# Kernel tuning notes

Measured on AMD Instinct MI355X. Metric: run time of the kernel, lower is better.

The kernel has to match this reference:

```python
import jax, jax.numpy as jnp
import numpy as np

DIM_IN = 512
DIM_OUT = 64


def setup_inputs() -> dict:
    key = jax.random.key(0)
    kx, kq, kk, kv = jax.random.split(key, 4)
    x = jax.random.normal(kx, (4, 4096, DIM_IN), dtype=jnp.float32)
    s = 1.0 / np.sqrt(DIM_IN)
    # torch nn.Linear stores weight as [out, in]; keep same convention
    Wq = jax.random.uniform(kq, (DIM_OUT, DIM_IN), jnp.float32, -s, s)
    Wk = jax.random.uniform(kk, (DIM_OUT, DIM_IN), jnp.float32, -s, s)
    Wv = jax.random.uniform(kv, (DIM_OUT, DIM_IN), jnp.float32, -s, s)
    return {"x": x, "Wq": Wq, "Wk": Wk, "Wv": Wv}


def reference(x, Wq, Wk, Wv):
    # q/k/v projections: [B,S,Din] @ [Din,Dout] -> [B,S,Dout]
    q = jnp.einsum("bsd,od->bso", x, Wq)
    k = jnp.einsum("bsd,od->bso", x, Wk)
    v = jnp.einsum("bsd,od->bso", x, Wv)
    scale = 1.0 / jnp.sqrt(jnp.asarray(q.shape[-1], q.dtype))
    scores = jnp.einsum("bqo,bko->bqk", q, k) * scale  # [B,S,S]
    weights = jax.nn.softmax(scores, axis=-1)
    out = jnp.einsum("bqk,bko->bqo", weights, v)  # [B,S,Dout]
    return out
```

## Files before the change

kernel.cpp:

```cpp
#include <hip/hip_runtime.h>
#include <hip/hip_bf16.h>

#define SEQ 4096
#define MTOT 16384

typedef float f32x4  __attribute__((ext_vector_type(4)));
typedef float f32x16 __attribute__((ext_vector_type(16)));
typedef _Float16 f16;
typedef _Float16 f16x4 __attribute__((ext_vector_type(4)));
typedef _Float16 f16x8 __attribute__((ext_vector_type(8)));
typedef unsigned int   u32;
typedef unsigned int   u32x2 __attribute__((ext_vector_type(2)));
typedef unsigned short u16;

static constexpr size_t QL_B   = 0;
static constexpr size_t KL_B   = 2u << 20;
static constexpr size_t VL_B   = 4u << 20;
static constexpr size_t WL_B   = 6u << 20;
static constexpr size_t PART_B = 8u << 20;
static constexpr size_t ML_B   = 42u << 20;

__device__ __forceinline__ u16 h16(float v) { return __builtin_bit_cast(u16, (f16)v); }
__device__ __forceinline__ u32 pkrtz(float a, float b) {
  return __builtin_bit_cast(u32, __builtin_amdgcn_cvt_pkrtz(a, b));
}
__device__ __forceinline__ void gl16(const u16* g, u16* l) {
  __builtin_amdgcn_global_load_lds((const __attribute__((address_space(1))) void*)g,
                                   (__attribute__((address_space(3))) void*)l, 16, 0, 0);
}

__global__ __launch_bounds__(256) void wconv_kernel(const float* __restrict__ Wq,
                                                    const float* __restrict__ Wk,
                                                    const float* __restrict__ Wv,
                                                    u16* __restrict__ wlin) {
  const float QSC = 0.18033688011112042f;
  int e = blockIdx.x * 256 + threadIdx.x;
  int flat = e * 4;
  int colg = flat >> 9;
  int k0   = flat & 511;
  int mat  = colg >> 6;
  const float* W = (mat == 0) ? Wq : (mat == 1 ? Wk : Wv);
  f32x4 v = *(const f32x4*)(W + (size_t)(colg & 63) * 512 + k0);
  if (mat == 0) v *= QSC;
  int s = colg >> 4, r16 = colg & 15;
  int step = k0 >> 5, g = (k0 & 31) >> 3, jb = k0 & 7;
  __attribute__((aligned(8))) u16 b[4];
#pragma unroll
  for (int j = 0; j < 4; ++j) b[j] = h16(v[j]);
  *(uint2*)(wlin + ((size_t)(s * 16 + step) * 64 + g * 16 + r16) * 8 + jb) = *(uint2*)b;
}

__global__ __launch_bounds__(256, 4) void proj_kernel(const float* __restrict__ x,
                                                      const u16* __restrict__ wlin,
                                                      u16* __restrict__ ws) {
  __shared__ __attribute__((aligned(16))) u16 xl[8192];
  float* scr = (float*)xl;

  const int tid  = threadIdx.x;
  const int blk  = blockIdx.x;
  const int lane = tid & 63;
  const int ng   = tid >> 6;
  const int r16  = lane & 15;
  const int g    = lane >> 4;
  const int m0   = blk * 16;

#pragma unroll
  for (int i = 0; i < 8; ++i) {
    int f = tid * 4 + i * 1024;
    int row = f >> 9, k0 = f & 511;
    f32x4 v = *(const f32x4*)(x + (size_t)m0 * 512 + f);
    __attribute__((aligned(8))) u16 b[4];
#pragma unroll
    for (int j = 0; j < 4; ++j) b[j] = h16(v[j]);
    int ln = ((k0 & 31) >> 3) * 16 + row;
    *(uint2*)(xl + ((size_t)(k0 >> 5) * 64 + ln) * 8 + (k0 & 7)) = *(uint2*)b;
  }
  __syncthreads();

  f32x4 acc[3];
#pragma unroll
  for (int s = 0; s < 3; ++s) acc[s] = (f32x4){0.f, 0.f, 0.f, 0.f};

#pragma unroll 2
  for (int step = 0; step < 16; ++step) {
    f16x8 a = *(const f16x8*)(xl + ((size_t)step * 64 + lane) * 8);
#pragma unroll
    for (int s = 0; s < 3; ++s) {
      int sg = ng * 3 + s;
      f16x8 b = *(const f16x8*)(wlin + ((size_t)(sg * 16 + step) * 64 + lane) * 8);
      acc[s] = __builtin_amdgcn_mfma_f32_16x16x32_f16(a, b, acc[s], 0, 0, 0);
    }
  }
  __syncthreads();

#pragma unroll
  for (int s = 0; s < 3; ++s)
#pragma unroll
    for (int rr = 0; rr < 4; ++rr)
      scr[(g * 4 + rr) * 193 + ng * 48 + s * 16 + r16] = acc[s][rr];
  __syncthreads();

  u16* Ql = ws + (QL_B >> 1);
  u16* Kl = ws + (KL_B >> 1);
  u16* Vl = ws + (VL_B >> 1);
  const int batch = m0 >> 12;
  const int tile  = (m0 >> 5) & 127;
  const int half  = (m0 >> 4) & 1;

  {
    int t2 = tid & 127;
    int r  = t2 & 15, hh = (t2 >> 4) & 1, ch = t2 >> 5;
    int l31 = half * 16 + r;
    __attribute__((aligned(16))) u16 b[8];
    if (tid < 128) {
#pragma unroll
      for (int j = 0; j < 8; ++j) b[j] = h16(scr[r * 193 + 64 + ch * 16 + hh * 8 + j]);
      *(uint4*)(Kl + ((size_t)((batch * 128 + tile) * 4 + ch) * 64 + hh * 32 + l31) * 8) =
          *(uint4*)b;
    } else {
#pragma unroll
      for (int j = 0; j < 8; ++j) b[j] = h16(scr[r * 193 + ch * 16 + hh * 8 + j]);
      int qhalf = (m0 >> 5);
      *(uint4*)(Ql + ((size_t)(qhalf * 4 + ch) * 64 + hh * 32 + l31) * 8) = *(uint4*)b;
    }
  }
  {
    int z = tid & 1, l31 = (tid >> 1) & 31, hh = (tid >> 6) & 1, db = tid >> 7;
    int d = db * 32 + l31;
    __attribute__((aligned(8))) u16 b[4];
#pragma unroll
    for (int j = 0; j < 4; ++j) b[j] = h16(scr[(8 * z + 4 * hh + j) * 193 + 128 + d]);
    *(uint2*)(Vl + ((size_t)(((batch * 128 + tile) * 2 + db) * 2 + half) * 64 + hh * 32 + l31) *
                       8 + z * 4) = *(uint2*)b;
  }
}

__global__ __launch_bounds__(512, 4) void attn_kernel(u16* __restrict__ ws) {
  __shared__ __attribute__((aligned(16))) u16 kvb[2][8192];

  const int tid  = threadIdx.x;
  const int w    = tid >> 6;
  const int lane = tid & 63;
  const int l31  = lane & 31;
  const int h    = lane >> 5;
  const int bx   = blockIdx.x;
  const int qb   = bx >> 3;
  const int sp   = bx & 7;
  const int bb   = qb >> 4;
  const int q0   = qb * 256 + w * 32;

  const u16* Ql = ws + (QL_B >> 1);
  const u16* Kl = ws + (KL_B >> 1);
  const u16* Vl = ws + (VL_B >> 1);

  const int qhalf = qb * 8 + w;
  f16x8 qf[4];
#pragma unroll
  for (int ch = 0; ch < 4; ++ch)
    qf[ch] = *(const f16x8*)(Ql + ((size_t)(qhalf * 4 + ch) * 64 + lane) * 8);

  f32x16 oacc[2];
#pragma unroll
  for (int db = 0; db < 2; ++db)
#pragma unroll
    for (int r = 0; r < 16; ++r) oacc[db][r] = 0.f;
  float mrun = -INFINITY, lrun = 0.f;
  const float RTHR = 11.0f;

  const int kt0 = bb * 128 + sp * 16;

  auto stage = [&](int b, int p) {
#pragma unroll
    for (int cc = 0; cc < 2; ++cc) {
      const int c = w * 2 + cc;
      const u16* src;
      if (c < 8) {
        src = Kl + (size_t)(kt0 + p * 2 + (c >> 2)) * 2048 + (c & 3) * 512 + lane * 8;
      } else {
        const int c2 = c - 8;
        src = Vl + (size_t)(kt0 + p * 2 + (c2 >> 2)) * 2048 + (c2 & 3) * 512 + lane * 8;
      }
      gl16(src, &kvb[b][c * 512]);
    }
  };

  stage(0, 0);
  __syncthreads();

#pragma unroll 1
  for (int p = 0; p < 8; ++p) {
    const int cur = p & 1;
    if (p < 7) stage(cur ^ 1, p + 1);

#pragma unroll
    for (int s = 0; s < 2; ++s) {
      f16x8 ka[4], vp[2][2];
#pragma unroll
      for (int ch = 0; ch < 4; ++ch)
        ka[ch] = *(const f16x8*)&kvb[cur][((s << 2) + ch) * 512 + lane * 8];
#pragma unroll
      for (int db = 0; db < 2; ++db)
#pragma unroll
        for (int pp = 0; pp < 2; ++pp)
          vp[db][pp] = *(const f16x8*)&kvb[cur][(8 + (s << 2) + db * 2 + pp) * 512 + lane * 8];

      f32x16 sac;
#pragma unroll
      for (int r = 0; r < 16; ++r) sac[r] = 0.f;
#pragma unroll
      for (int ch = 0; ch < 4; ++ch)
        sac = __builtin_amdgcn_mfma_f32_32x32x16_f16(ka[ch], qf[ch], sac, 0, 0, 0);

      float mt = sac[0];
#pragma unroll
      for (int r = 1; r < 16; ++r) mt = fmaxf(mt, sac[r]);
      if (__any(mt > mrun + RTHR)) {
        float mtw  = fmaxf(mt, __shfl_xor(mt, 32));
        float nm   = fmaxf(mrun, mtw);
        float corr = exp2f(mrun - nm);
        lrun *= corr;
        mrun = nm;
#pragma unroll
        for (int db = 0; db < 2; ++db)
#pragma unroll
          for (int r = 0; r < 16; ++r) oacc[db][r] *= corr;
      }
#pragma unroll
      for (int r = 0; r < 16; ++r) {
        float pv = exp2f(sac[r] - mrun);
        sac[r] = pv;
        lrun += pv;
      }

      f16x4 pb[4];
#pragma unroll
      for (int c = 0; c < 4; ++c) {
        u32x2 pk;
        pk[0] = pkrtz(sac[4 * c + 0], sac[4 * c + 1]);
        pk[1] = pkrtz(sac[4 * c + 2], sac[4 * c + 3]);
        pb[c] = __builtin_bit_cast(f16x4, pk);
      }

#pragma unroll
      for (int db = 0; db < 2; ++db)
#pragma unroll
        for (int pp = 0; pp < 2; ++pp) {
          f16x4 vlo = __builtin_shufflevector(vp[db][pp], vp[db][pp], 0, 1, 2, 3);
          f16x4 vhi = __builtin_shufflevector(vp[db][pp], vp[db][pp], 4, 5, 6, 7);
          oacc[db] = __builtin_amdgcn_mfma_f32_32x32x8f16(vlo, pb[2 * pp], oacc[db], 0, 0, 0);
          oacc[db] = __builtin_amdgcn_mfma_f32_32x32x8f16(vhi, pb[2 * pp + 1], oacc[db], 0, 0, 0);
        }
    }
    __syncthreads();
  }

  lrun += __shfl_xor(lrun, 32);

  float* Op = (float*)((char*)ws + PART_B) + (size_t)sp * MTOT * 64;
#pragma unroll
  for (int db = 0; db < 2; ++db)
#pragma unroll
    for (int r = 0; r < 16; ++r) {
      int d = db * 32 + (r & 3) + 8 * (r >> 2) + 4 * h;
      Op[(size_t)(q0 + l31) * 64 + d] = oacc[db][r];
    }
  if (h == 0) {
    float* Mm = (float*)((char*)ws + ML_B);
    float* Ll = Mm + 8 * MTOT;
    Mm[(size_t)sp * MTOT + q0 + l31] = mrun;
    Ll[(size_t)sp * MTOT + q0 + l31] = lrun;
  }
}

__global__ __launch_bounds__(256) void merge_kernel(const u16* __restrict__ ws,
                                                    float* __restrict__ out) {
  int gid = blockIdx.x * 256 + threadIdx.x;
  int row = gid >> 2, dg = gid & 3;
  const float* Mm = (const float*)((const char*)ws + ML_B);
  const float* Ll = Mm + 8 * MTOT;
  float mv[8];
  float mg = -INFINITY;
#pragma unroll
  for (int i = 0; i < 8; ++i) {
    mv[i] = Mm[(size_t)i * MTOT + row];
    mg = fmaxf(mg, mv[i]);
  }
  float den = 0.f, wv[8];
#pragma unroll
  for (int i = 0; i < 8; ++i) {
    wv[i] = exp2f(mv[i] - mg);
    den += wv[i] * Ll[(size_t)i * MTOT + row];
  }
  f32x4 acc[4];
#pragma unroll
  for (int m = 0; m < 4; ++m) acc[m] = (f32x4){0.f, 0.f, 0.f, 0.f};
  const float* Op = (const float*)((const char*)ws + PART_B);
#pragma unroll
  for (int i = 0; i < 8; ++i)
#pragma unroll
    for (int m = 0; m < 4; ++m) {
      f32x4 t = *(const f32x4*)(Op + ((size_t)i * MTOT + row) * 64 + dg * 16 + m * 4);
      acc[m] += wv[i] * t;
    }
  float inv = 1.f / den;
#pragma unroll
  for (int m = 0; m < 4; ++m) {
    f32x4 r = acc[m] * inv;
    *(f32x4*)(out + (size_t)row * 64 + dg * 16 + m * 4) = r;
  }
}

extern "C" void kernel_launch(void* const* d_in, const int* in_sizes, int n_in,
                              void* d_out, int out_size, void* d_ws, size_t ws_size,
                              hipStream_t stream) {
  const float* x  = (const float*)d_in[0];
  const float* Wq = (const float*)d_in[1];
  const float* Wk = (const float*)d_in[2];
  const float* Wv = (const float*)d_in[3];
  u16* ws = (u16*)d_ws;
  (void)in_sizes; (void)n_in; (void)out_size; (void)ws_size;

  wconv_kernel<<<96, 256, 0, stream>>>(Wq, Wk, Wv, ws + (WL_B >> 1));
  proj_kernel<<<1024, 256, 0, stream>>>(x, ws + (WL_B >> 1), ws);
  attn_kernel<<<512, 512, 0, stream>>>(ws);
  merge_kernel<<<256, 256, 0, stream>>>(ws, (float*)d_out);
}
```

Baseline: 64.69 us.

## Process two query tiles per wave in attention, halving block size

Each wave now handles 64 query rows as two 32-row tiles, so every K/V fragment read from shared memory feeds twice as many MFMAs. Blocks shrink from 512 to 256 threads, and each wave stages four chunks instead of two. Partial outputs are written as float4 vectors instead of scalar stores. The cost is higher register pressure from doubled accumulators and Q fragments, and fewer waves per block to hide latency.

```diff
diff --git a/kernel.cpp b/kernel.cpp
--- a/kernel.cpp
+++ b/kernel.cpp
@@ -135,7 +135,7 @@
   }
 }
 
-__global__ __launch_bounds__(512, 4) void attn_kernel(u16* __restrict__ ws) {
+__global__ __launch_bounds__(256, 2) void attn_kernel(u16* __restrict__ ws) {
   __shared__ __attribute__((aligned(16))) u16 kvb[2][8192];
 
   const int tid  = threadIdx.x;
@@ -147,32 +147,37 @@
   const int qb   = bx >> 3;
   const int sp   = bx & 7;
   const int bb   = qb >> 4;
-  const int q0   = qb * 256 + w * 32;
+  const int q0   = qb * 256 + w * 64;
 
   const u16* Ql = ws + (QL_B >> 1);
   const u16* Kl = ws + (KL_B >> 1);
   const u16* Vl = ws + (VL_B >> 1);
 
-  const int qhalf = qb * 8 + w;
-  f16x8 qf[4];
-#pragma unroll
-  for (int ch = 0; ch < 4; ++ch)
-    qf[ch] = *(const f16x8*)(Ql + ((size_t)(qhalf * 4 + ch) * 64 + lane) * 8);
-
-  f32x16 oacc[2];
+  f16x8 qf[2][4];
+#pragma unroll
+  for (int qk = 0; qk < 2; ++qk)
+#pragma unroll
+    for (int ch = 0; ch < 4; ++ch)
+      qf[qk][ch] =
+          *(const f16x8*)(Ql + ((size_t)((qb * 8 + w * 2 + qk) * 4 + ch) * 64 + lane) * 8);
+
+  f32x16 oacc[2][2];
 #pragma unroll
   for (int db = 0; db < 2; ++db)
 #pragma unroll
-    for (int r = 0; r < 16; ++r) oacc[db][r] = 0.f;
-  float mrun = -INFINITY, lrun = 0.f;
+    for (int qk = 0; qk < 2; ++qk)
+#pragma unroll
+      for (int r = 0; r < 16; ++r) oacc[db][qk][r] = 0.f;
+  float mrun[2] = {-INFINITY, -INFINITY};
+  float lrun[2] = {0.f, 0.f};
   const float RTHR = 11.0f;
 
   const int kt0 = bb * 128 + sp * 16;
 
   auto stage = [&](int b, int p) {
 #pragma unroll
-    for (int cc = 0; cc < 2; ++cc) {
-      const int c = w * 2 + cc;
+    for (int cc = 0; cc < 4; ++cc) {
+      const int c = w * 4 + cc;
       const u16* src;
       if (c < 8) {
         src = Kl + (size_t)(kt0 + p * 2 + (c >> 2)) * 2048 + (c & 3) * 512 + lane * 8;
@@ -204,41 +209,47 @@
         for (int pp = 0; pp < 2; ++pp)
           vp[db][pp] = *(const f16x8*)&kvb[cur][(8 + (s << 2) + db * 2 + pp) * 512 + lane * 8];
 
-      f32x16 sac;
-#pragma unroll
-      for (int r = 0; r < 16; ++r) sac[r] = 0.f;
-#pragma unroll
-      for (int ch = 0; ch < 4; ++ch)
-        sac = __builtin_amdgcn_mfma_f32_32x32x16_f16(ka[ch], qf[ch], sac, 0, 0, 0);
-
-      float mt = sac[0];
-#pragma unroll
-      for (int r = 1; r < 16; ++r) mt = fmaxf(mt, sac[r]);
-      if (__any(mt > mrun + RTHR)) {
-        float mtw  = fmaxf(mt, __shfl_xor(mt, 32));
-        float nm   = fmaxf(mrun, mtw);
-        float corr = exp2f(mrun - nm);
-        lrun *= corr;
-        mrun = nm;
-#pragma unroll
-        for (int db = 0; db < 2; ++db)
-#pragma unroll
-          for (int r = 0; r < 16; ++r) oacc[db][r] *= corr;
-      }
-#pragma unroll
-      for (int r = 0; r < 16; ++r) {
-        float pv = exp2f(sac[r] - mrun);
-        sac[r] = pv;
-        lrun += pv;
-      }
-
-      f16x4 pb[4];
-#pragma unroll
-      for (int c = 0; c < 4; ++c) {
-        u32x2 pk;
-        pk[0] = pkrtz(sac[4 * c + 0], sac[4 * c + 1]);
-        pk[1] = pkrtz(sac[4 * c + 2], sac[4 * c + 3]);
-        pb[c] = __builtin_bit_cast(f16x4, pk);
+      f32x16 sac[2];
+#pragma unroll
+      for (int qk = 0; qk < 2; ++qk)
+#pragma unroll
+        for (int r = 0; r < 16; ++r) sac[qk][r] = 0.f;
+#pragma unroll
+      for (int qk = 0; qk < 2; ++qk)
+#pragma unroll
+        for (int ch = 0; ch < 4; ++ch)
+          sac[qk] = __builtin_amdgcn_mfma_f32_32x32x16_f16(ka[ch], qf[qk][ch], sac[qk], 0, 0, 0);
+
+      f16x4 pb[2][4];
+#pragma unroll
+      for (int qk = 0; qk < 2; ++qk) {
+        float mt = sac[qk][0];
+#pragma unroll
+        for (int r = 1; r < 16; ++r) mt = fmaxf(mt, sac[qk][r]);
+        if (__any(mt > mrun[qk] + RTHR)) {
+          float mtw  = fmaxf(mt, __shfl_xor(mt, 32));
+          float nm   = fmaxf(mrun[qk], mtw);
+          float corr = exp2f(mrun[qk] - nm);
+          lrun[qk] *= corr;
+          mrun[qk] = nm;
+#pragma unroll
+          for (int db = 0; db < 2; ++db)
+#pragma unroll
+            for (int r = 0; r < 16; ++r) oacc[db][qk][r] *= corr;
+        }
+#pragma unroll
+        for (int r = 0; r < 16; ++r) {
+          float pv = exp2f(sac[qk][r] - mrun[qk]);
+          sac[qk][r] = pv;
+          lrun[qk] += pv;
+        }
+#pragma unroll
+        for (int c = 0; c < 4; ++c) {
+          u32x2 pk;
+          pk[0] = pkrtz(sac[qk][4 * c + 0], sac[qk][4 * c + 1]);
+          pk[1] = pkrtz(sac[qk][4 * c + 2], sac[qk][4 * c + 3]);
+          pb[qk][c] = __builtin_bit_cast(f16x4, pk);
+        }
       }
 
 #pragma unroll
@@ -247,28 +258,40 @@
         for (int pp = 0; pp < 2; ++pp) {
           f16x4 vlo = __builtin_shufflevector(vp[db][pp], vp[db][pp], 0, 1, 2, 3);
           f16x4 vhi = __builtin_shufflevector(vp[db][pp], vp[db][pp], 4, 5, 6, 7);
-          oacc[db] = __builtin_amdgcn_mfma_f32_32x32x8f16(vlo, pb[2 * pp], oacc[db], 0, 0, 0);
-          oacc[db] = __builtin_amdgcn_mfma_f32_32x32x8f16(vhi, pb[2 * pp + 1], oacc[db], 0, 0, 0);
+#pragma unroll
+          for (int qk = 0; qk < 2; ++qk) {
+            oacc[db][qk] =
+                __builtin_amdgcn_mfma_f32_32x32x8f16(vlo, pb[qk][2 * pp], oacc[db][qk], 0, 0, 0);
+            oacc[db][qk] = __builtin_amdgcn_mfma_f32_32x32x8f16(vhi, pb[qk][2 * pp + 1],
+                                                                oacc[db][qk], 0, 0, 0);
+          }
         }
     }
     __syncthreads();
   }
 
-  lrun += __shfl_xor(lrun, 32);
+#pragma unroll
+  for (int qk = 0; qk < 2; ++qk) lrun[qk] += __shfl_xor(lrun[qk], 32);
 
   float* Op = (float*)((char*)ws + PART_B) + (size_t)sp * MTOT * 64;
 #pragma unroll
   for (int db = 0; db < 2; ++db)
 #pragma unroll
-    for (int r = 0; r < 16; ++r) {
-      int d = db * 32 + (r & 3) + 8 * (r >> 2) + 4 * h;
-      Op[(size_t)(q0 + l31) * 64 + d] = oacc[db][r];
-    }
+    for (int qk = 0; qk < 2; ++qk)
+#pragma unroll
+      for (int g = 0; g < 4; ++g) {
+        f32x4 v = {oacc[db][qk][4 * g + 0], oacc[db][qk][4 * g + 1],
+                   oacc[db][qk][4 * g + 2], oacc[db][qk][4 * g + 3]};
+        *(f32x4*)(Op + (size_t)(q0 + qk * 32 + l31) * 64 + db * 32 + 8 * g + 4 * h) = v;
+      }
   if (h == 0) {
     float* Mm = (float*)((char*)ws + ML_B);
     float* Ll = Mm + 8 * MTOT;
-    Mm[(size_t)sp * MTOT + q0 + l31] = mrun;
-    Ll[(size_t)sp * MTOT + q0 + l31] = lrun;
+#pragma unroll
+    for (int qk = 0; qk < 2; ++qk) {
+      Mm[(size_t)sp * MTOT + q0 + qk * 32 + l31] = mrun[qk];
+      Ll[(size_t)sp * MTOT + q0 + qk * 32 + l31] = lrun[qk];
+    }
   }
 }
 
@@ -322,6 +345,6 @@
 
   wconv_kernel<<<96, 256, 0, stream>>>(Wq, Wk, Wv, ws + (WL_B >> 1));
   proj_kernel<<<1024, 256, 0, stream>>>(x, ws + (WL_B >> 1), ws);
-  attn_kernel<<<512, 512, 0, stream>>>(ws);
+  attn_kernel<<<512, 256, 0, stream>>>(ws);
   merge_kernel<<<256, 256, 0, stream>>>(ws, (float*)d_out);
 }
```

Measured after the change: 65.52 us. About the same (+1.3%).
